# Kernel optimization log

Measured on AMD Instinct MI355X. Metric: run time of the kernel, lower is better.

The kernel has to match this reference:

```python
import jax, jax.numpy as jnp
import numpy as np
from jax.scipy.special import logsumexp

D, V, B, N = 256, 10000, 16, 22
CF, CR, CA = 400, 120, 48   # num_func_cats, num_res_cats, num_arg_cats
NEG = -1e9


def setup_inputs() -> dict:
    key = jax.random.key(0)
    ks = jax.random.split(key, 12)
    s = 0.1
    return {
        "fake_emb": jnp.eye(CR, dtype=jnp.float32),  # nn.Parameter(torch.eye(num_res_cats))
        "nt_emb": jax.random.normal(ks[0], (CF, D), jnp.float32),
        "rule_W": jax.random.normal(ks[1], (2 * CA, CR), jnp.float32) * s,
        "rule_b": jnp.zeros((2 * CA,), jnp.float32),
        "root_w": jax.random.normal(ks[2], (CF,), jnp.float32) * s,  # root_mlp weight (input dim 1)
        "root_b": jnp.zeros((CF,), jnp.float32),
        "root_mask": jnp.zeros((CF,), jnp.float32),  # can_be_root mask (0 = allowed)
        "split_W1": jax.random.normal(ks[3], (D, D), jnp.float32) * s,
        "split_b1": jnp.zeros((D,), jnp.float32),
        "res_W": jax.random.normal(ks[4], (2, 2, D, D), jnp.float32) * s,  # 2 ResidualLayers x 2 Linears
        "res_b": jnp.zeros((2, 2, D), jnp.float32),
        "split_Wo": jax.random.normal(ks[5], (D, 2), jnp.float32) * s,
        "split_bo": jnp.zeros((2,), jnp.float32),
        "emit_W": jax.random.normal(ks[6], (D, V), jnp.float32) * s,  # word emission head
        "emit_b": jnp.zeros((V,), jnp.float32),
        "words": jax.random.randint(ks[7], (B, N), 0, V),
        "lfunc_ixs": jax.random.randint(ks[8], (CR, CA), 0, CF),
        "rfunc_ixs": jax.random.randint(ks[9], (CR, CA), 0, CF),
    }


def reference(fake_emb, nt_emb, rule_W, rule_b, root_w, root_b, root_mask,
              split_W1, split_b1, res_W, res_b, split_Wo, split_bo,
              emit_W, emit_b, words, lfunc_ixs, rfunc_ixs):
    # ---- grammar scores (set_grammar branch) ----
    # root_mlp(eye(1)).squeeze() == root_w + root_b
    root_scores = jax.nn.log_softmax(root_mask + root_w + root_b)          # [CF]
    rule_scores = jax.nn.log_softmax(fake_emb @ rule_W.T + rule_b, axis=1)  # [CR, 2*CA]

    # split_mlp: Linear -> ResidualLayer x2 -> Linear(D,2)
    h = nt_emb @ split_W1 + split_b1
    for i in range(2):  # fixed small layer loop
        t = jax.nn.relu(h @ res_W[i, 0] + res_b[i, 0])
        h = jax.nn.relu(t @ res_W[i, 1] + res_b[i, 1]) + h
    split_scores = jax.nn.log_softmax(h @ split_Wo + split_bo, axis=1)      # [CF, 2]

    gL = rule_scores[:, :CA] + split_scores[:CR, 0:1]  # full_G_larg [CR, CA]
    gR = rule_scores[:, CA:] + split_scores[:CR, 0:1]  # full_G_rarg [CR, CA]

    # ---- emission model: log p(word | category) gathered per token ----
    word_lp = jax.nn.log_softmax(nt_emb @ emit_W + emit_b, axis=-1)  # [CF, V]
    emit = word_lp[:, words]                                         # [CF, B, N]
    term = (split_scores[:, 1][:, None, None] + emit).transpose(2, 1, 0)  # [N, B, CF]

    # ---- CKY inside pass: beta[i, j, b, cat] over spans ----
    beta = jnp.full((N, N, B, CF), NEG, jnp.float32)
    d = jnp.arange(N)
    beta = beta.at[d, d].set(term)

    for w in range(2, N + 1):  # recurrence over span widths (static)
        S = N - w + 1
        st = np.arange(S)[:, None]          # span starts [S,1]
        kk = np.arange(1, w)[None, :]       # split points [1,w-1]
        left = beta[st, st + kk - 1]                                   # [S,w-1,B,CF]
        right = beta[st + kk, np.broadcast_to(st + w - 1, (S, w - 1))]  # [S,w-1,B,CF]
        # res -> arg(left) + rfunc(right)
        sL = gL + left[..., :CA][..., None, :] + right[..., rfunc_ixs]  # [S,w-1,B,CR,CA]
        # res -> lfunc(left) + arg(right)
        sR = gR + left[..., lfunc_ixs] + right[..., :CA][..., None, :]
        new = jnp.logaddexp(logsumexp(sL, axis=(1, 4)),
                            logsumexp(sR, axis=(1, 4)))                 # [S,B,CR]
        full = jnp.full((S, B, CF), NEG, jnp.float32).at[..., :CR].set(new)
        beta = beta.at[st[:, 0], st[:, 0] + w - 1].set(full)

    ll = logsumexp(root_scores + beta[0, N - 1], axis=-1)  # [B]
    return -ll  # logprob_list * -1
```

## Files before the change

kernel.cpp:

```cpp
#include <hip/hip_runtime.h>
#include <math.h>

#define D 256
#define V 10000
#define BB 16
#define NN 22
#define CF 400
#define CR 120
#define CA 48
#define CRP 121
#define PADF 20

__global__ __launch_bounds__(512) void k_mlp(const float* __restrict__ nt_emb, const float* __restrict__ W1,
                      const float* __restrict__ b1, const float* __restrict__ resW,
                      const float* __restrict__ resb, const float* __restrict__ Wo,
                      const float* __restrict__ bo, float* __restrict__ split_scores) {
  __shared__ float xs[2][D], hs[2][D], ts[2][D], prt[2][2][D];
  __shared__ float redg[2][4][2];
  int t = threadIdx.x; int c = t & 255; int h = t >> 8;
  int f0 = blockIdx.x * 2;
  xs[h][c] = nt_emb[(size_t)(f0 + h) * D + c];
  __syncthreads();
  int d0 = h * 128;
  float a0 = 0.f, a1 = 0.f;
#pragma unroll 8
  for (int dd = 0; dd < 128; dd++) {
    float wv = W1[(size_t)(d0 + dd) * D + c];
    a0 += xs[0][d0 + dd] * wv; a1 += xs[1][d0 + dd] * wv;
  }
  prt[0][h][c] = a0; prt[1][h][c] = a1;
  __syncthreads();
  if (h == 0) {
    float bv = b1[c];
    hs[0][c] = prt[0][0][c] + prt[0][1][c] + bv;
    hs[1][c] = prt[1][0][c] + prt[1][1][c] + bv;
  }
  __syncthreads();
  for (int il = 0; il < 2; il++) {
    const float* W = resW + (size_t)(il * 2) * D * D;
    a0 = 0.f; a1 = 0.f;
#pragma unroll 8
    for (int dd = 0; dd < 128; dd++) {
      float wv = W[(size_t)(d0 + dd) * D + c];
      a0 += hs[0][d0 + dd] * wv; a1 += hs[1][d0 + dd] * wv;
    }
    prt[0][h][c] = a0; prt[1][h][c] = a1;
    __syncthreads();
    if (h == 0) {
      float bv = resb[(il * 2) * D + c];
      ts[0][c] = fmaxf(prt[0][0][c] + prt[0][1][c] + bv, 0.f);
      ts[1][c] = fmaxf(prt[1][0][c] + prt[1][1][c] + bv, 0.f);
    }
    __syncthreads();
    const float* W2 = resW + (size_t)(il * 2 + 1) * D * D;
    a0 = 0.f; a1 = 0.f;
#pragma unroll 8
    for (int dd = 0; dd < 128; dd++) {
      float wv = W2[(size_t)(d0 + dd) * D + c];
      a0 += ts[0][d0 + dd] * wv; a1 += ts[1][d0 + dd] * wv;
    }
    prt[0][h][c] = a0; prt[1][h][c] = a1;
    __syncthreads();
    if (h == 0) {
      float bv = resb[(il * 2 + 1) * D + c];
      hs[0][c] = fmaxf(prt[0][0][c] + prt[0][1][c] + bv, 0.f) + hs[0][c];
      hs[1][c] = fmaxf(prt[1][0][c] + prt[1][1][c] + bv, 0.f) + hs[1][c];
    }
    __syncthreads();
  }
  float y0 = hs[h][c] * Wo[c * 2 + 0], y1 = hs[h][c] * Wo[c * 2 + 1];
  for (int off = 32; off; off >>= 1) { y0 += __shfl_down(y0, off, 64); y1 += __shfl_down(y1, off, 64); }
  int wq = (t >> 6) & 3;
  if ((t & 63) == 0) { redg[h][wq][0] = y0; redg[h][wq][1] = y1; }
  __syncthreads();
  if (c == 0) {
    float s0 = redg[h][0][0] + redg[h][1][0] + redg[h][2][0] + redg[h][3][0] + bo[0];
    float s1 = redg[h][0][1] + redg[h][1][1] + redg[h][2][1] + redg[h][3][1] + bo[1];
    float m = fmaxf(s0, s1);
    float z = m + __logf(__expf(s0 - m) + __expf(s1 - m));
    split_scores[(f0 + h) * 2 + 0] = s0 - z;
    split_scores[(f0 + h) * 2 + 1] = s1 - z;
  }
}

#define RT 8
__global__ __launch_bounds__(128) void k_emit_partial(const float* __restrict__ nt_emb,
                               const float* __restrict__ emit_W,
                               const float* __restrict__ emit_b, float* __restrict__ partial) {
  __shared__ float xs[RT][D];
  __shared__ float ldsw[RT][2];
  int t = threadIdx.x;
  int f0 = blockIdx.x * RT;
  int v0 = blockIdx.y * 512 + t * 4;
  for (int idx = t; idx < RT * D; idx += 128) {
    int ri = idx >> 8, d = idx & 255;
    xs[ri][d] = nt_emb[(size_t)(f0 + ri) * D + d];
  }
  __syncthreads();
  float psum[RT];
  for (int ri = 0; ri < RT; ri++) psum[ri] = 0.f;
  if (v0 < V) {
    float acc[RT][4];
#pragma unroll
    for (int ri = 0; ri < RT; ri++)
      for (int j = 0; j < 4; j++) acc[ri][j] = 0.f;
    for (int d4 = 0; d4 < D / 4; d4++) {
      float4 w0 = *(const float4*)(emit_W + (size_t)(4 * d4 + 0) * V + v0);
      float4 w1 = *(const float4*)(emit_W + (size_t)(4 * d4 + 1) * V + v0);
      float4 w2 = *(const float4*)(emit_W + (size_t)(4 * d4 + 2) * V + v0);
      float4 w3 = *(const float4*)(emit_W + (size_t)(4 * d4 + 3) * V + v0);
#pragma unroll
      for (int ri = 0; ri < RT; ri++) {
        float4 xv = *(const float4*)(&xs[ri][4 * d4]);
        acc[ri][0] += xv.x * w0.x + xv.y * w1.x + xv.z * w2.x + xv.w * w3.x;
        acc[ri][1] += xv.x * w0.y + xv.y * w1.y + xv.z * w2.y + xv.w * w3.y;
        acc[ri][2] += xv.x * w0.z + xv.y * w1.z + xv.z * w2.z + xv.w * w3.z;
        acc[ri][3] += xv.x * w0.w + xv.y * w1.w + xv.z * w2.w + xv.w * w3.w;
      }
    }
    float4 eb = *(const float4*)(emit_b + v0);
#pragma unroll
    for (int ri = 0; ri < RT; ri++)
      psum[ri] = __expf(acc[ri][0] + eb.x) + __expf(acc[ri][1] + eb.y) +
                 __expf(acc[ri][2] + eb.z) + __expf(acc[ri][3] + eb.w);
  }
  int lane = t & 63, wid = t >> 6;
  for (int ri = 0; ri < RT; ri++) {
    float v = psum[ri];
    for (int off = 32; off; off >>= 1) v += __shfl_down(v, off, 64);
    if (lane == 0) ldsw[ri][wid] = v;
  }
  __syncthreads();
  if (t < RT) partial[(f0 + t) * 32 + blockIdx.y] = ldsw[t][0] + ldsw[t][1];
}

__global__ void k_glgr(const float* __restrict__ rule_W, const float* __restrict__ rule_b,
                       const float* __restrict__ split_scores,
                       const int* __restrict__ lf, const int* __restrict__ rf,
                       const float* __restrict__ partialE, float* __restrict__ logZ,
                       float4* __restrict__ rules) {
  __shared__ float red[128];
  __shared__ float shv[96];
  int r = blockIdx.x;
  int t = threadIdx.x;
  if (r == CR) {
    for (int f = t; f < CF; f += 128) {
      float s = 0.f;
      for (int ct = 0; ct < 20; ct++) s += partialE[f * 32 + ct];
      logZ[f] = __logf(s);
    }
    return;
  }
  float x = (t < 96) ? (rule_W[t * CR + r] + rule_b[t]) : -INFINITY;
  red[t] = x; __syncthreads();
  for (int off = 64; off; off >>= 1) { if (t < off) red[t] = fmaxf(red[t], red[t + off]); __syncthreads(); }
  float m = red[0]; __syncthreads();
  red[t] = (t < 96) ? __expf(x - m) : 0.f; __syncthreads();
  for (int off = 64; off; off >>= 1) { if (t < off) red[t] += red[t + off]; __syncthreads(); }
  float z = m + __logf(red[0]);
  float s0 = split_scores[r * 2 + 0];
  if (t < 96) shv[t] = __expf((x - z) + s0);
  __syncthreads();
  if (t < CA) {
    float4 pk;
    pk.x = shv[t];
    pk.y = shv[CA + t];
    pk.z = __int_as_float(rf[r * CA + t]);
    pk.w = __int_as_float(lf[r * CA + t]);
    rules[r * CA + t] = pk;
  }
}

__global__ __launch_bounds__(512) void k_term(const float* __restrict__ nt_emb,
                       const float* __restrict__ emit_W,
                       const float* __restrict__ emit_b, const int* __restrict__ words,
                       const float* __restrict__ split_scores, const float* __restrict__ logZ,
                       float* __restrict__ ET, float* __restrict__ bmax) {
  __shared__ float vals[CF];
  __shared__ float redw[8];
  __shared__ float mfin;
  int blk = blockIdx.x;
  int b = blk / NN, n = blk % NN;
  int t = threadIdx.x;
  int lane = t & 63, wid = t >> 6;
  int wd = words[b * NN + n];
  float wc0 = emit_W[(size_t)(4 * lane + 0) * V + wd];
  float wc1 = emit_W[(size_t)(4 * lane + 1) * V + wd];
  float wc2 = emit_W[(size_t)(4 * lane + 2) * V + wd];
  float wc3 = emit_W[(size_t)(4 * lane + 3) * V + wd];
  float eb = emit_b[wd];
  float vmax = -INFINITY;
  int fbase = wid * 50;
  for (int k = 0; k < 50; k += 2) {
    int f0 = fbase + k, f1 = f0 + 1;
    float4 xa = *(const float4*)(nt_emb + (size_t)f0 * D + 4 * lane);
    float4 xb = *(const float4*)(nt_emb + (size_t)f1 * D + 4 * lane);
    float va = xa.x * wc0 + xa.y * wc1 + xa.z * wc2 + xa.w * wc3;
    float vb = xb.x * wc0 + xb.y * wc1 + xb.z * wc2 + xb.w * wc3;
    for (int off = 32; off; off >>= 1) {
      va += __shfl_down(va, off, 64);
      vb += __shfl_down(vb, off, 64);
    }
    if (lane == 0) {
      float fa = split_scores[f0 * 2 + 1] + (va + eb) - logZ[f0];
      float fb = split_scores[f1 * 2 + 1] + (vb + eb) - logZ[f1];
      vals[f0] = fa; vals[f1] = fb;
      vmax = fmaxf(vmax, fmaxf(fa, fb));
    }
  }
  if (lane == 0) redw[wid] = vmax;
  __syncthreads();
  if (t == 0) {
    float m = redw[0];
    for (int i2 = 1; i2 < 8; i2++) m = fmaxf(m, redw[i2]);
    mfin = m;
    bmax[(n * NN + n) * BB + b] = m;
  }
  __syncthreads();
  float m = mfin;
  for (int f = t; f < CF; f += 512) ET[((size_t)n * CF + f) * BB + b] = __expf(vals[f] - m);
}

__global__ __launch_bounds__(512) void k_cky_part(const float4* __restrict__ rules,
                      const float* __restrict__ ET, const float* __restrict__ EB,
                      const float* __restrict__ bmax, float* __restrict__ partial,
                      int w, int rsplit) {
  __shared__ float SL[CF * PADF];
  __shared__ float SR[CF * PADF];
  __shared__ float sMbuf[21 * BB];
  __shared__ float cks[BB];
  __shared__ float4 sred[512];
  int t = threadIdx.x;
  int blk = blockIdx.x;
  int rb = blk % rsplit; int rem = blk / rsplit;
  int wm1 = w - 1;
  int k = rem % wm1; int s = rem / wm1;
  int i = s, j = s + w - 1;
  bool ld = (k == 0), rd = (k == wm1 - 1);
  if (t < BB * wm1) {
    int k2 = t >> 4, b2 = t & 15;
    sMbuf[t] = bmax[(i * NN + (i + k2)) * BB + b2] + bmax[((i + k2 + 1) * NN + j) * BB + b2];
  }
  __syncthreads();
  if (t < BB) {
    float M = sMbuf[t];
    for (int k2 = 1; k2 < wm1; k2++) M = fmaxf(M, sMbuf[k2 * BB + t]);
    cks[t] = __expf(sMbuf[k * BB + t] - M);
  }
  const float* srcL = ld ? (ET + (size_t)i * CF * BB) : (EB + (size_t)(i * NN + (i + k)) * CRP * BB);
  const float* srcR = rd ? (ET + (size_t)j * CF * BB) : (EB + (size_t)((i + k + 1) * NN + j) * CRP * BB);
  int rowsL = ld ? CF : CRP, rowsR = rd ? CF : CRP;
  for (int idx = t; idx < rowsL * 4; idx += 512) {
    int f = idx >> 2, q = idx & 3;
    *(float4*)&SL[f * PADF + q * 4] = *(const float4*)&srcL[f * BB + q * 4];
  }
  for (int idx = t; idx < rowsR * 4; idx += 512) {
    int f = idx >> 2, q = idx & 3;
    *(float4*)&SR[f * PADF + q * 4] = *(const float4*)&srcR[f * BB + q * 4];
  }
  __syncthreads();
  int nr = CR / rsplit;
  int asplit = 128 / nr;
  int bq = t & 3, rr = t >> 2;
  float4 acc = {0.f, 0.f, 0.f, 0.f};
  bool act = (rr < nr * asplit);
  int rloc = rr % nr, asub = rr / nr;
  int r = rb * nr + rloc;
  if (act) {
    int na = CA / asplit;
    const float4* rp = rules + (size_t)r * CA + asub * na;
    int boff = bq * 4;
    int aB = asub * na;
#pragma unroll 4
    for (int a0 = 0; a0 < na; a0++) {
      float4 rule = rp[a0];
      int a = aB + a0;
      int fL = __float_as_int(rule.z);
      int fR = __float_as_int(rule.w);
      int fLc = rd ? fL : min(fL, 120);
      int fRc = ld ? fR : min(fR, 120);
      float4 La = *(const float4*)&SL[a * PADF + boff];
      float4 Ra = *(const float4*)&SR[a * PADF + boff];
      float4 Rg = *(const float4*)&SR[fLc * PADF + boff];
      float4 Lg = *(const float4*)&SL[fRc * PADF + boff];
      acc.x += rule.x * (La.x * Rg.x) + rule.y * (Lg.x * Ra.x);
      acc.y += rule.x * (La.y * Rg.y) + rule.y * (Lg.y * Ra.y);
      acc.z += rule.x * (La.z * Rg.z) + rule.y * (Lg.z * Ra.z);
      acc.w += rule.x * (La.w * Rg.w) + rule.y * (Lg.w * Ra.w);
    }
  }
  if (asplit > 1) {
    sred[t] = acc;
    __syncthreads();
    if (act && asub == 0) {
      for (int s2 = 1; s2 < asplit; s2++) {
        float4 o = sred[t + s2 * nr * 4];
        acc.x += o.x; acc.y += o.y; acc.z += o.z; acc.w += o.w;
      }
    }
  }
  if (act && asub == 0) {
    float4 c4 = *(const float4*)&cks[bq * 4];
    acc.x *= c4.x; acc.y *= c4.y; acc.z *= c4.z; acc.w *= c4.w;
    *(float4*)&partial[(((size_t)s * 21 + k) * CR + r) * BB + bq * 4] = acc;
  }
}

__global__ __launch_bounds__(512) void k_cky_comb(const float* __restrict__ partial,
                      float* __restrict__ EB, float* __restrict__ bmax, int w) {
  __shared__ float sums[CR * BB];
  __shared__ float sMbuf[21 * BB];
  __shared__ float msum[BB];
  __shared__ float Mb[BB];
  int t = threadIdx.x;
  int s = blockIdx.x;
  int i = s, j = s + w - 1;
  int wm1 = w - 1;
  if (t < BB * wm1) {
    int k2 = t >> 4, b2 = t & 15;
    sMbuf[t] = bmax[(i * NN + (i + k2)) * BB + b2] + bmax[((i + k2 + 1) * NN + j) * BB + b2];
  }
  __syncthreads();
  if (t < BB) {
    float M = sMbuf[t];
    for (int k2 = 1; k2 < wm1; k2++) M = fmaxf(M, sMbuf[k2 * BB + t]);
    Mb[t] = M;
  }
  int bq = t & 3, rr = t >> 2;
  float4 sum = {0.f, 0.f, 0.f, 0.f};
  if (rr < CR) {
    for (int k2 = 0; k2 < wm1; k2++) {
      float4 p = *(const float4*)&partial[(((size_t)s * 21 + k2) * CR + rr) * BB + bq * 4];
      sum.x += p.x; sum.y += p.y; sum.z += p.z; sum.w += p.w;
    }
    *(float4*)&sums[rr * BB + bq * 4] = sum;
  }
  __syncthreads();
  if (t < BB) {
    float m = 0.f;
    for (int r2 = 0; r2 < CR; r2++) m = fmaxf(m, sums[r2 * BB + t]);
    m = fmaxf(m, 1e-35f);
    msum[t] = m;
    bmax[(i * NN + j) * BB + t] = Mb[t] + __logf(m);
  }
  __syncthreads();
  if (rr < CR) {
    float4 m4 = *(const float4*)&msum[bq * 4];
    sum.x /= m4.x; sum.y /= m4.y; sum.z /= m4.z; sum.w /= m4.w;
    *(float4*)&EB[(((size_t)i * NN + j) * CRP + rr) * BB + bq * 4] = sum;
  }
  if (t < BB) EB[(((size_t)i * NN + j) * CRP + 120) * BB + t] = 0.f;
}

__global__ __launch_bounds__(128) void k_final(const float* __restrict__ root_w,
                        const float* __restrict__ root_b, const float* __restrict__ root_mask,
                        const float* __restrict__ EB, const float* __restrict__ bmax,
                        float* __restrict__ out) {
  __shared__ float red[128];
  int b = blockIdx.x;
  int t = threadIdx.x;
  float xv[4];
  float lm = -INFINITY;
  for (int kq = 0; kq < 4; kq++) {
    int f = t + kq * 128;
    xv[kq] = (f < CF) ? (root_mask[f] + root_w[f] + root_b[f]) : -INFINITY;
    lm = fmaxf(lm, xv[kq]);
  }
  red[t] = lm; __syncthreads();
  for (int off = 64; off; off >>= 1) { if (t < off) red[t] = fmaxf(red[t], red[t + off]); __syncthreads(); }
  float M = red[0]; __syncthreads();
  float le = 0.f;
  for (int kq = 0; kq < 4; kq++) le += (t + kq * 128 < CF) ? __expf(xv[kq] - M) : 0.f;
  red[t] = le; __syncthreads();
  for (int off = 64; off; off >>= 1) { if (t < off) red[t] += red[t + off]; __syncthreads(); }
  float z = M + __logf(red[0]);
  __syncthreads();
  float x = (t < CR) ? __expf(xv[0] - z) * EB[(((size_t)0 * NN + (NN - 1)) * CRP + t) * BB + b] : 0.f;
  red[t] = x; __syncthreads();
  for (int off = 64; off; off >>= 1) { if (t < off) red[t] += red[t + off]; __syncthreads(); }
  if (t == 0) out[b] = -(bmax[(0 * NN + (NN - 1)) * BB + b] + __logf(red[0]));
}

extern "C" void kernel_launch(void* const* d_in, const int* in_sizes, int n_in,
                              void* d_out, int out_size, void* d_ws, size_t ws_size,
                              hipStream_t stream) {
  const float* nt_emb   = (const float*)d_in[1];
  const float* rule_W   = (const float*)d_in[2];
  const float* rule_b   = (const float*)d_in[3];
  const float* root_w   = (const float*)d_in[4];
  const float* root_b   = (const float*)d_in[5];
  const float* root_mask= (const float*)d_in[6];
  const float* split_W1 = (const float*)d_in[7];
  const float* split_b1 = (const float*)d_in[8];
  const float* res_W    = (const float*)d_in[9];
  const float* res_b    = (const float*)d_in[10];
  const float* split_Wo = (const float*)d_in[11];
  const float* split_bo = (const float*)d_in[12];
  const float* emit_W   = (const float*)d_in[13];
  const float* emit_b   = (const float*)d_in[14];
  const int*   words    = (const int*)d_in[15];
  const int*   lfunc    = (const int*)d_in[16];
  const int*   rfunc    = (const int*)d_in[17];

  float* ws = (float*)d_ws;
  float* ET           = ws;
  float* EB           = ET + NN * CF * BB;
  float* bmaxbuf      = EB + NN * NN * CRP * BB;
  float* partialK     = bmaxbuf + NN * NN * BB;
  float* rules        = partialK + 21 * 21 * CR * BB;
  float* split_scores = rules + CR * CA * 4;
  float* logZ         = split_scores + 2 * CF;
  float* partialE     = logZ + CF;

  hipLaunchKernelGGL(k_mlp, dim3(CF / 2), dim3(512), 0, stream, nt_emb, split_W1, split_b1,
                     res_W, res_b, split_Wo, split_bo, split_scores);
  hipLaunchKernelGGL(k_emit_partial, dim3(CF / RT, 20), dim3(128), 0, stream, nt_emb, emit_W, emit_b, partialE);
  hipLaunchKernelGGL(k_glgr, dim3(CR + 1), dim3(128), 0, stream, rule_W, rule_b, split_scores,
                     lfunc, rfunc, partialE, logZ, (float4*)rules);
  hipLaunchKernelGGL(k_term, dim3(BB * NN), dim3(512), 0, stream, nt_emb, emit_W, emit_b,
                     words, split_scores, logZ, ET, bmaxbuf);
  for (int w = 2; w <= NN; w++) {
    int S = NN - w + 1;
    int units = S * (w - 1);
    int rsplit = (units >= 224) ? 1 : ((units >= 112) ? 2 : 4);
    hipLaunchKernelGGL(k_cky_part, dim3(units * rsplit), dim3(512), 0, stream,
                       (const float4*)rules, ET, EB, bmaxbuf, partialK, w, rsplit);
    hipLaunchKernelGGL(k_cky_comb, dim3(S), dim3(512), 0, stream, partialK, EB, bmaxbuf, w);
  }
  hipLaunchKernelGGL(k_final, dim3(BB), dim3(128), 0, stream, root_w, root_b, root_mask,
                     EB, bmaxbuf, (float*)d_out);
}
```

Before: 370.4 us.

## Fuse split MLP and emission partial-sum kernels; split small CKY widths further

Merges the split-score MLP and the emission log-partition partial sums into one launch. Blocks below MLPB run the MLP and the remaining blocks run the emission partial sums, so both run concurrently and one kernel launch is saved. The emission part is retiled to 512-thread blocks covering 2048 vocab columns each, which cuts the partial-sum count per category from 20 to 5; k_glgr is updated to read the new layout. For the widest CKY spans, where there are few work units, the rule dimension is now split 8 ways to expose more parallelism, at the cost of more partial results to combine.

```diff
diff --git a/kernel.cpp b/kernel.cpp
--- a/kernel.cpp
+++ b/kernel.cpp
@@ -11,127 +11,136 @@
 #define CRP 121
 #define PADF 20
 
-__global__ __launch_bounds__(512) void k_mlp(const float* __restrict__ nt_emb, const float* __restrict__ W1,
-                      const float* __restrict__ b1, const float* __restrict__ resW,
-                      const float* __restrict__ resb, const float* __restrict__ Wo,
-                      const float* __restrict__ bo, float* __restrict__ split_scores) {
-  __shared__ float xs[2][D], hs[2][D], ts[2][D], prt[2][2][D];
-  __shared__ float redg[2][4][2];
-  int t = threadIdx.x; int c = t & 255; int h = t >> 8;
-  int f0 = blockIdx.x * 2;
-  xs[h][c] = nt_emb[(size_t)(f0 + h) * D + c];
-  __syncthreads();
-  int d0 = h * 128;
-  float a0 = 0.f, a1 = 0.f;
-#pragma unroll 8
-  for (int dd = 0; dd < 128; dd++) {
-    float wv = W1[(size_t)(d0 + dd) * D + c];
-    a0 += xs[0][d0 + dd] * wv; a1 += xs[1][d0 + dd] * wv;
-  }
-  prt[0][h][c] = a0; prt[1][h][c] = a1;
-  __syncthreads();
-  if (h == 0) {
-    float bv = b1[c];
-    hs[0][c] = prt[0][0][c] + prt[0][1][c] + bv;
-    hs[1][c] = prt[1][0][c] + prt[1][1][c] + bv;
-  }
-  __syncthreads();
-  for (int il = 0; il < 2; il++) {
-    const float* W = resW + (size_t)(il * 2) * D * D;
-    a0 = 0.f; a1 = 0.f;
+#define RT 8
+#define MLPB 200
+__global__ __launch_bounds__(512) void k_mlp_emit(const float* __restrict__ nt_emb,
+                      const float* __restrict__ W1, const float* __restrict__ b1,
+                      const float* __restrict__ resW, const float* __restrict__ resb,
+                      const float* __restrict__ Wo, const float* __restrict__ bo,
+                      const float* __restrict__ emit_W, const float* __restrict__ emit_b,
+                      float* __restrict__ split_scores, float* __restrict__ partial) {
+  int bid = blockIdx.x;
+  int t = threadIdx.x;
+  if (bid < MLPB) {
+    __shared__ float xs[2][D], hs[2][D], ts[2][D], prt[2][2][D];
+    __shared__ float redg[2][4][2];
+    int c = t & 255; int h = t >> 8;
+    int f0 = bid * 2;
+    xs[h][c] = nt_emb[(size_t)(f0 + h) * D + c];
+    __syncthreads();
+    int d0 = h * 128;
+    float a0 = 0.f, a1 = 0.f;
 #pragma unroll 8
     for (int dd = 0; dd < 128; dd++) {
-      float wv = W[(size_t)(d0 + dd) * D + c];
-      a0 += hs[0][d0 + dd] * wv; a1 += hs[1][d0 + dd] * wv;
+      float wv = W1[(size_t)(d0 + dd) * D + c];
+      a0 += xs[0][d0 + dd] * wv; a1 += xs[1][d0 + dd] * wv;
     }
     prt[0][h][c] = a0; prt[1][h][c] = a1;
     __syncthreads();
     if (h == 0) {
-      float bv = resb[(il * 2) * D + c];
-      ts[0][c] = fmaxf(prt[0][0][c] + prt[0][1][c] + bv, 0.f);
-      ts[1][c] = fmaxf(prt[1][0][c] + prt[1][1][c] + bv, 0.f);
-    }
-    __syncthreads();
-    const float* W2 = resW + (size_t)(il * 2 + 1) * D * D;
-    a0 = 0.f; a1 = 0.f;
+      float bv = b1[c];
+      hs[0][c] = prt[0][0][c] + prt[0][1][c] + bv;
+      hs[1][c] = prt[1][0][c] + prt[1][1][c] + bv;
+    }
+    __syncthreads();
+    for (int il = 0; il < 2; il++) {
+      const float* W = resW + (size_t)(il * 2) * D * D;
+      a0 = 0.f; a1 = 0.f;
 #pragma unroll 8
-    for (int dd = 0; dd < 128; dd++) {
-      float wv = W2[(size_t)(d0 + dd) * D + c];
-      a0 += ts[0][d0 + dd] * wv; a1 += ts[1][d0 + dd] * wv;
-    }
-    prt[0][h][c] = a0; prt[1][h][c] = a1;
-    __syncthreads();
-    if (h == 0) {
-      float bv = resb[(il * 2 + 1) * D + c];
-      hs[0][c] = fmaxf(prt[0][0][c] + prt[0][1][c] + bv, 0.f) + hs[0][c];
-      hs[1][c] = fmaxf(prt[1][0][c] + prt[1][1][c] + bv, 0.f) + hs[1][c];
-    }
-    __syncthreads();
-  }
-  float y0 = hs[h][c] * Wo[c * 2 + 0], y1 = hs[h][c] * Wo[c * 2 + 1];
-  for (int off = 32; off; off >>= 1) { y0 += __shfl_down(y0, off, 64); y1 += __shfl_down(y1, off, 64); }
-  int wq = (t >> 6) & 3;
-  if ((t & 63) == 0) { redg[h][wq][0] = y0; redg[h][wq][1] = y1; }
-  __syncthreads();
-  if (c == 0) {
-    float s0 = redg[h][0][0] + redg[h][1][0] + redg[h][2][0] + redg[h][3][0] + bo[0];
-    float s1 = redg[h][0][1] + redg[h][1][1] + redg[h][2][1] + redg[h][3][1] + bo[1];
-    float m = fmaxf(s0, s1);
-    float z = m + __logf(__expf(s0 - m) + __expf(s1 - m));
-    split_scores[(f0 + h) * 2 + 0] = s0 - z;
-    split_scores[(f0 + h) * 2 + 1] = s1 - z;
-  }
-}
-
-#define RT 8
-__global__ __launch_bounds__(128) void k_emit_partial(const float* __restrict__ nt_emb,
-                               const float* __restrict__ emit_W,
-                               const float* __restrict__ emit_b, float* __restrict__ partial) {
-  __shared__ float xs[RT][D];
-  __shared__ float ldsw[RT][2];
-  int t = threadIdx.x;
-  int f0 = blockIdx.x * RT;
-  int v0 = blockIdx.y * 512 + t * 4;
-  for (int idx = t; idx < RT * D; idx += 128) {
-    int ri = idx >> 8, d = idx & 255;
-    xs[ri][d] = nt_emb[(size_t)(f0 + ri) * D + d];
-  }
-  __syncthreads();
-  float psum[RT];
-  for (int ri = 0; ri < RT; ri++) psum[ri] = 0.f;
-  if (v0 < V) {
-    float acc[RT][4];
+      for (int dd = 0; dd < 128; dd++) {
+        float wv = W[(size_t)(d0 + dd) * D + c];
+        a0 += hs[0][d0 + dd] * wv; a1 += hs[1][d0 + dd] * wv;
+      }
+      prt[0][h][c] = a0; prt[1][h][c] = a1;
+      __syncthreads();
+      if (h == 0) {
+        float bv = resb[(il * 2) * D + c];
+        ts[0][c] = fmaxf(prt[0][0][c] + prt[0][1][c] + bv, 0.f);
+        ts[1][c] = fmaxf(prt[1][0][c] + prt[1][1][c] + bv, 0.f);
+      }
+      __syncthreads();
+      const float* W2 = resW + (size_t)(il * 2 + 1) * D * D;
+      a0 = 0.f; a1 = 0.f;
+#pragma unroll 8
+      for (int dd = 0; dd < 128; dd++) {
+        float wv = W2[(size_t)(d0 + dd) * D + c];
+        a0 += ts[0][d0 + dd] * wv; a1 += ts[1][d0 + dd] * wv;
+      }
+      prt[0][h][c] = a0; prt[1][h][c] = a1;
+      __syncthreads();
+      if (h == 0) {
+        float bv = resb[(il * 2 + 1) * D + c];
+        hs[0][c] = fmaxf(prt[0][0][c] + prt[0][1][c] + bv, 0.f) + hs[0][c];
+        hs[1][c] = fmaxf(prt[1][0][c] + prt[1][1][c] + bv, 0.f) + hs[1][c];
+      }
+      __syncthreads();
+    }
+    float y0 = hs[h][c] * Wo[c * 2 + 0], y1 = hs[h][c] * Wo[c * 2 + 1];
+    for (int off = 32; off; off >>= 1) { y0 += __shfl_down(y0, off, 64); y1 += __shfl_down(y1, off, 64); }
+    int wq = (t >> 6) & 3;
+    if ((t & 63) == 0) { redg[h][wq][0] = y0; redg[h][wq][1] = y1; }
+    __syncthreads();
+    if (c == 0) {
+      float s0 = redg[h][0][0] + redg[h][1][0] + redg[h][2][0] + redg[h][3][0] + bo[0];
+      float s1 = redg[h][0][1] + redg[h][1][1] + redg[h][2][1] + redg[h][3][1] + bo[1];
+      float m = fmaxf(s0, s1);
+      float z = m + __logf(__expf(s0 - m) + __expf(s1 - m));
+      split_scores[(f0 + h) * 2 + 0] = s0 - z;
+      split_scores[(f0 + h) * 2 + 1] = s1 - z;
+    }
+  } else {
+    __shared__ float exs[RT][D];
+    __shared__ float ldsw[RT][8];
+    int e = bid - MLPB;
+    int y = e / 50;
+    int xt = e % 50;
+    int f0 = xt * RT;
+    int v0 = y * 2048 + t * 4;
+    for (int idx = t; idx < RT * D; idx += 512) {
+      int ri = idx >> 8, d = idx & 255;
+      exs[ri][d] = nt_emb[(size_t)(f0 + ri) * D + d];
+    }
+    __syncthreads();
+    float psum[RT];
+    for (int ri = 0; ri < RT; ri++) psum[ri] = 0.f;
+    if (v0 < V) {
+      float acc[RT][4];
 #pragma unroll
-    for (int ri = 0; ri < RT; ri++)
-      for (int j = 0; j < 4; j++) acc[ri][j] = 0.f;
-    for (int d4 = 0; d4 < D / 4; d4++) {
-      float4 w0 = *(const float4*)(emit_W + (size_t)(4 * d4 + 0) * V + v0);
-      float4 w1 = *(const float4*)(emit_W + (size_t)(4 * d4 + 1) * V + v0);
-      float4 w2 = *(const float4*)(emit_W + (size_t)(4 * d4 + 2) * V + v0);
-      float4 w3 = *(const float4*)(emit_W + (size_t)(4 * d4 + 3) * V + v0);
+      for (int ri = 0; ri < RT; ri++)
+        for (int j = 0; j < 4; j++) acc[ri][j] = 0.f;
+      for (int d4 = 0; d4 < D / 4; d4++) {
+        float4 w0 = *(const float4*)(emit_W + (size_t)(4 * d4 + 0) * V + v0);
+        float4 w1 = *(const float4*)(emit_W + (size_t)(4 * d4 + 1) * V + v0);
+        float4 w2 = *(const float4*)(emit_W + (size_t)(4 * d4 + 2) * V + v0);
+        float4 w3 = *(const float4*)(emit_W + (size_t)(4 * d4 + 3) * V + v0);
 #pragma unroll
-      for (int ri = 0; ri < RT; ri++) {
-        float4 xv = *(const float4*)(&xs[ri][4 * d4]);
-        acc[ri][0] += xv.x * w0.x + xv.y * w1.x + xv.z * w2.x + xv.w * w3.x;
-        acc[ri][1] += xv.x * w0.y + xv.y * w1.y + xv.z * w2.y + xv.w * w3.y;
-        acc[ri][2] += xv.x * w0.z + xv.y * w1.z + xv.z * w2.z + xv.w * w3.z;
-        acc[ri][3] += xv.x * w0.w + xv.y * w1.w + xv.z * w2.w + xv.w * w3.w;
-      }
-    }
-    float4 eb = *(const float4*)(emit_b + v0);
+        for (int ri = 0; ri < RT; ri++) {
+          float4 xv = *(const float4*)(&exs[ri][4 * d4]);
+          acc[ri][0] += xv.x * w0.x + xv.y * w1.x + xv.z * w2.x + xv.w * w3.x;
+          acc[ri][1] += xv.x * w0.y + xv.y * w1.y + xv.z * w2.y + xv.w * w3.y;
+          acc[ri][2] += xv.x * w0.z + xv.y * w1.z + xv.z * w2.z + xv.w * w3.z;
+          acc[ri][3] += xv.x * w0.w + xv.y * w1.w + xv.z * w2.w + xv.w * w3.w;
+        }
+      }
+      float4 eb = *(const float4*)(emit_b + v0);
 #pragma unroll
-    for (int ri = 0; ri < RT; ri++)
-      psum[ri] = __expf(acc[ri][0] + eb.x) + __expf(acc[ri][1] + eb.y) +
-                 __expf(acc[ri][2] + eb.z) + __expf(acc[ri][3] + eb.w);
-  }
-  int lane = t & 63, wid = t >> 6;
-  for (int ri = 0; ri < RT; ri++) {
-    float v = psum[ri];
-    for (int off = 32; off; off >>= 1) v += __shfl_down(v, off, 64);
-    if (lane == 0) ldsw[ri][wid] = v;
-  }
-  __syncthreads();
-  if (t < RT) partial[(f0 + t) * 32 + blockIdx.y] = ldsw[t][0] + ldsw[t][1];
+      for (int ri = 0; ri < RT; ri++)
+        psum[ri] = __expf(acc[ri][0] + eb.x) + __expf(acc[ri][1] + eb.y) +
+                   __expf(acc[ri][2] + eb.z) + __expf(acc[ri][3] + eb.w);
+    }
+    int lane = t & 63, wid = t >> 6;
+    for (int ri = 0; ri < RT; ri++) {
+      float v = psum[ri];
+      for (int off = 32; off; off >>= 1) v += __shfl_down(v, off, 64);
+      if (lane == 0) ldsw[ri][wid] = v;
+    }
+    __syncthreads();
+    if (t < RT) {
+      float s = 0.f;
+      for (int wv = 0; wv < 8; wv++) s += ldsw[t][wv];
+      partial[(f0 + t) * 8 + y] = s;
+    }
+  }
 }
 
 __global__ void k_glgr(const float* __restrict__ rule_W, const float* __restrict__ rule_b,
@@ -146,7 +155,7 @@
   if (r == CR) {
     for (int f = t; f < CF; f += 128) {
       float s = 0.f;
-      for (int ct = 0; ct < 20; ct++) s += partialE[f * 32 + ct];
+      for (int ct = 0; ct < 5; ct++) s += partialE[f * 8 + ct];
       logZ[f] = __logf(s);
     }
     return;
@@ -412,9 +421,9 @@
   float* logZ         = split_scores + 2 * CF;
   float* partialE     = logZ + CF;
 
-  hipLaunchKernelGGL(k_mlp, dim3(CF / 2), dim3(512), 0, stream, nt_emb, split_W1, split_b1,
-                     res_W, res_b, split_Wo, split_bo, split_scores);
-  hipLaunchKernelGGL(k_emit_partial, dim3(CF / RT, 20), dim3(128), 0, stream, nt_emb, emit_W, emit_b, partialE);
+  hipLaunchKernelGGL(k_mlp_emit, dim3(MLPB + 250), dim3(512), 0, stream, nt_emb,
+                     split_W1, split_b1, res_W, res_b, split_Wo, split_bo,
+                     emit_W, emit_b, split_scores, partialE);
   hipLaunchKernelGGL(k_glgr, dim3(CR + 1), dim3(128), 0, stream, rule_W, rule_b, split_scores,
                      lfunc, rfunc, partialE, logZ, (float4*)rules);
   hipLaunchKernelGGL(k_term, dim3(BB * NN), dim3(512), 0, stream, nt_emb, emit_W, emit_b,
@@ -422,7 +431,7 @@
   for (int w = 2; w <= NN; w++) {
     int S = NN - w + 1;
     int units = S * (w - 1);
-    int rsplit = (units >= 224) ? 1 : ((units >= 112) ? 2 : 4);
+    int rsplit = (units >= 224) ? 1 : ((units >= 112) ? 2 : ((units >= 56) ? 4 : 8));
     hipLaunchKernelGGL(k_cky_part, dim3(units * rsplit), dim3(512), 0, stream,
                        (const float4*)rules, ET, EB, bmaxbuf, partialK, w, rsplit);
     hipLaunchKernelGGL(k_cky_comb, dim3(S), dim3(512), 0, stream, partialK, EB, bmaxbuf, w);
```

Result: faster. 349.3 us (-5.7%).
